# Kernel tuning notes

Hardware: AMD Instinct MI355X
Metric: run time of the kernel (lower is better)

## Reference

```python
import jax, jax.numpy as jnp
import numpy as np

B, L, E, H = 4, 2048, 1024, 16
DK = E // H


def setup_inputs() -> dict:
    key = jax.random.key(0)
    k1, k2, k3 = jax.random.split(key, 3)
    x = jax.random.normal(k1, (B, L, E), dtype=jnp.float32)
    # torch Linear weights are [out, in]; xavier-ish scaling
    w_qkv = jax.random.normal(k2, (3 * E, E), dtype=jnp.float32) * (2.0 / (E + 3 * E)) ** 0.5
    wo = jax.random.normal(k3, (E, E), dtype=jnp.float32) * (1.0 / E) ** 0.5
    # causal mask: scores filled with -inf where mask == 0
    mask = jnp.tril(jnp.ones((L, L), dtype=bool))
    return {"x": x, "mask": mask, "w_qkv": w_qkv, "wo": wo}


def reference(x, mask, w_qkv, wo):
    b, l, e = x.shape
    # qkv projection: Linear with weight [3E, E] -> x @ W^T
    qkv = x @ w_qkv.T                              # [b, l, 3E]
    qkv = qkv.reshape(b, l, 3, H, DK)              # (three h d) split
    q = jnp.transpose(qkv[:, :, 0], (0, 2, 1, 3))  # [b, h, l, d]
    k = jnp.transpose(qkv[:, :, 1], (0, 2, 1, 3))
    v = jnp.transpose(qkv[:, :, 2], (0, 2, 1, 3))
    scores = jnp.einsum('bhld,bhmd->bhlm', q, k) / np.sqrt(DK)  # [b, h, l, l]
    scores = jnp.where(mask, scores, -jnp.inf)
    attn = jax.nn.softmax(scores, axis=-1)
    out = jnp.einsum('bhlm,bhmd->bhld', attn, v)   # [b, h, l, d]
    out = jnp.transpose(out, (0, 2, 1, 3)).reshape(b, l, e)  # b l (h d)
    return out @ wo.T
```

## Files before the change

### kernel.cpp

```cpp
#include <hip/hip_runtime.h>
#include <stdint.h>


typedef __bf16 bf16;
typedef __bf16 bf16x4 __attribute__((ext_vector_type(4)));
typedef __bf16 bf16x8 __attribute__((ext_vector_type(8)));
typedef float floatx4 __attribute__((ext_vector_type(4)));
typedef short s16x4 __attribute__((ext_vector_type(4)));

#define MFMA32(a, b, c) __builtin_amdgcn_mfma_f32_16x16x32_bf16(a, b, c, 0, 0, 0)
#define MFMA16(a, b, c) __builtin_amdgcn_mfma_f32_16x16x16bf16_1k(a, b, c, 0, 0, 0)

typedef const __attribute__((address_space(1))) uint32_t* gas_t;
typedef __attribute__((address_space(3))) uint32_t* las_t;

__device__ __forceinline__ void async16(void* lds, const void* g) {
  __builtin_amdgcn_global_load_lds((gas_t)g, (las_t)lds, 16, 0, 0);
}

__global__ void cvt_all(const float4* __restrict__ x, const float4* __restrict__ wq,
                        const float4* __restrict__ wo, bf16x4* __restrict__ xb,
                        bf16x4* __restrict__ wqb, bf16x4* __restrict__ wob) {
  const int NX = 2097152, NQ = 786432;
  int i = blockIdx.x * blockDim.x + threadIdx.x;
  float4 v;
  bf16x4* dst;
  int j;
  if (i < NX) { j = i; v = x[j]; dst = xb; }
  else if (i < NX + NQ) { j = i - NX; v = wq[j]; dst = wqb; }
  else { j = i - NX - NQ; v = wo[j]; dst = wob; }
  bf16x4 o;
  o[0] = (bf16)v.x; o[1] = (bf16)v.y; o[2] = (bf16)v.z; o[3] = (bf16)v.w;
  dst[j] = o;
}

template <int MODE>
__global__ __launch_bounds__(256) void gemm_bt(
    const bf16* __restrict__ A, const bf16* __restrict__ B,
    float* __restrict__ Cf, bf16* __restrict__ Qb, bf16* __restrict__ Kb,
    bf16* __restrict__ Vt, int M, int N, int K) {
  __shared__ __align__(16) bf16 smem[128 * 136];
  bf16* As = smem;
  bf16* Bs = smem + 128 * 32;
  const int tid = threadIdx.x;
  const int wave = tid >> 6, lane = tid & 63;
  const int wm = wave & 1, wn = wave >> 1;
  const int row0 = blockIdx.y * 128, col0 = blockIdx.x * 128;
  const int l15 = lane & 15, quad = lane >> 4;
  const int srow = lane >> 2;
  const int scol = (lane & 3) * 8;

  floatx4 acc[4][4] = {};

  for (int k0 = 0; k0 < K; k0 += 32) {
#pragma unroll
    for (int i = 0; i < 2; ++i) {
      int c = wave + i * 4;
      async16(&As[c * 512], A + (size_t)(row0 + c * 16 + srow) * K + k0 + scol);
      async16(&Bs[c * 512], B + (size_t)(col0 + c * 16 + srow) * K + k0 + scol);
    }
    __syncthreads();
    bf16x8 af[4], bfr[4];
#pragma unroll
    for (int t = 0; t < 4; ++t) {
      af[t]  = *(const bf16x8*)&As[(wm * 64 + t * 16 + l15) * 32 + quad * 8];
      bfr[t] = *(const bf16x8*)&Bs[(wn * 64 + t * 16 + l15) * 32 + quad * 8];
    }
#pragma unroll
    for (int mt = 0; mt < 4; ++mt)
#pragma unroll
      for (int nt = 0; nt < 4; ++nt)
        acc[mt][nt] = MFMA32(af[mt], bfr[nt], acc[mt][nt]);
    __syncthreads();
  }

  if (MODE == 1 && col0 >= 2048) {
#pragma unroll
    for (int mt = 0; mt < 4; ++mt)
#pragma unroll
      for (int nt = 0; nt < 4; ++nt) {
        int nl = wn * 64 + nt * 16 + l15;
        int ll = wm * 64 + mt * 16 + quad * 4;
        bf16x4 t;
#pragma unroll
        for (int r = 0; r < 4; ++r) t[r] = (bf16)acc[mt][nt][r];
        *(bf16x4*)&smem[nl * 136 + ll] = t;
      }
    __syncthreads();
    const int bb = row0 >> 11, l_base = row0 & 2047, hd0 = col0 - 2048;
#pragma unroll
    for (int it = 0; it < 8; ++it) {
      int rowi = it * 16 + (tid >> 4);
      int li = (tid & 15) * 8;
      bf16x8 v = *(const bf16x8*)&smem[rowi * 136 + li];
      int hd = hd0 + rowi;
      *(bf16x8*)&Vt[((((size_t)bb * 16 + (hd >> 6)) * 64 + (hd & 63)) << 11) +
                    l_base + li] = v;
    }
    return;
  }

#pragma unroll
  for (int mt = 0; mt < 4; ++mt)
#pragma unroll
    for (int nt = 0; nt < 4; ++nt)
#pragma unroll
      for (int r = 0; r < 4; ++r) {
        int gr = row0 + wm * 64 + mt * 16 + quad * 4 + r;
        int gc = col0 + wn * 64 + nt * 16 + l15;
        float v = acc[mt][nt][r];
        if (MODE == 2) {
          Cf[(size_t)gr * N + gc] = v;
        } else {
          int t = gc >> 10, hd = gc & 1023;
          if (t == 0) Qb[(size_t)gr * 1024 + hd] = (bf16)v;
          else        Kb[(size_t)gr * 1024 + hd] = (bf16)v;
        }
      }
}

__global__ __launch_bounds__(256) void gemm2_64(
    const bf16* __restrict__ A, const bf16* __restrict__ B,
    float* __restrict__ Cf, int M, int N, int K) {
  __shared__ __align__(16) bf16 As[64 * 32];
  __shared__ __align__(16) bf16 Bs[128 * 32];
  const int tid = threadIdx.x;
  const int wave = tid >> 6, lane = tid & 63;
  const int row0 = blockIdx.y * 64, col0 = blockIdx.x * 128;
  const int l15 = lane & 15, quad = lane >> 4;
  const int srow = lane >> 2, scol = (lane & 3) * 8;

  floatx4 acc[4][2] = {};

  for (int k0 = 0; k0 < K; k0 += 32) {
#pragma unroll
    for (int i = 0; i < 3; ++i) {
      int c = wave * 3 + i;
      if (c < 4)
        async16(&As[c * 512], A + (size_t)(row0 + c * 16 + srow) * K + k0 + scol);
      else
        async16(&Bs[(c - 4) * 512],
                B + (size_t)(col0 + (c - 4) * 16 + srow) * K + k0 + scol);
    }
    __syncthreads();
    bf16x8 af[4], bfr[2];
#pragma unroll
    for (int t = 0; t < 4; ++t)
      af[t] = *(const bf16x8*)&As[(t * 16 + l15) * 32 + quad * 8];
#pragma unroll
    for (int t = 0; t < 2; ++t)
      bfr[t] = *(const bf16x8*)&Bs[(wave * 32 + t * 16 + l15) * 32 + quad * 8];
#pragma unroll
    for (int mt = 0; mt < 4; ++mt)
#pragma unroll
      for (int nt = 0; nt < 2; ++nt)
        acc[mt][nt] = MFMA32(af[mt], bfr[nt], acc[mt][nt]);
    __syncthreads();
  }

#pragma unroll
  for (int mt = 0; mt < 4; ++mt)
#pragma unroll
    for (int nt = 0; nt < 2; ++nt)
#pragma unroll
      for (int r = 0; r < 4; ++r) {
        int gr = row0 + mt * 16 + quad * 4 + r;
        int gc = col0 + wave * 32 + nt * 16 + l15;
        Cf[(size_t)gr * N + gc] = acc[mt][nt][r];
      }
}

__global__ __launch_bounds__(256, 2) void flash_attn(
    const bf16* __restrict__ Qb, const bf16* __restrict__ Kb,
    const bf16* __restrict__ Vt, bf16* __restrict__ Ob) {
  const int bid0 = blockIdx.x;
  const int xcd = bid0 & 7, jj = bid0 >> 3;
  const int bh = xcd * 8 + (jj & 7);
  const int pr = jj >> 3;
  const int b = bh >> 4, h = bh & 15;
  const int tid = threadIdx.x;
  const int wave = tid >> 6, lane = tid & 63;
  const int l15 = lane & 15, quad = lane >> 4;

  const int qA = pr, qB = 31 - pr;

  __shared__ __align__(16) bf16 Ks2[2 * 64 * 64];
  __shared__ __align__(16) bf16 Vs2[2 * 64 * 64];

  const size_t x_base = (size_t)b * 2048 * 1024 + (size_t)h * 64;
  const size_t vt_base = (size_t)bh * 64 * 2048;

  const int k_lr = lane >> 3, k_c = lane & 7;

  auto stage = [&](int kt, int bufsel) {
    bf16* Kd = Ks2 + bufsel * 4096;
    bf16* Vd = Vs2 + bufsel * 4096;
#pragma unroll
    for (int i = 0; i < 2; ++i) {
      int o8 = wave * 2 + i;
      int row = o8 * 8 + k_lr;
      int sw = (k_c ^ (row & 7)) << 3;
      async16(&Kd[o8 * 512],
              Kb + x_base + (size_t)(kt * 64 + row) * 1024 + sw);
      async16(&Vd[o8 * 512],
              Vt + vt_base + (size_t)row * 2048 + kt * 64 + sw);
    }
  };

  auto load_q = [&](int q64, bf16x8* qf) {
#pragma unroll
    for (int ks = 0; ks < 2; ++ks) {
      const bf16* p = Qb + x_base +
          (size_t)(q64 * 64 + wave * 16 + l15) * 1024 + ks * 32 + quad * 8;
      bf16x8 v = *(const bf16x8*)p;
#pragma unroll
      for (int j = 0; j < 8; ++j) v[j] = (bf16)((float)v[j] * 0.18033688f);
      qf[ks] = v;
    }
  };

  stage(0, 0);

  bf16x8 qfA[2], qfB[2];
  load_q(qA, qfA);
  load_q(qB, qfB);

  floatx4 oA[4] = {}, oB[4] = {};
  float lA = 0.f, lB = 0.f;

  auto process = [&](const bf16x8* qf, floatx4* o, float& l_run,
                     int kt, int q64, bool diag, const bf16* Ks, const bf16* Vs) {
    floatx4 s[4] = {};
    __builtin_amdgcn_s_setprio(1);
#pragma unroll
    for (int nt = 0; nt < 4; ++nt) {
      int krow = nt * 16 + l15;
#pragma unroll
      for (int ks = 0; ks < 2; ++ks) {
        bf16x8 kf = *(const bf16x8*)&Ks[krow * 64 +
            ((((ks << 2) | quad) ^ (l15 & 7)) << 3)];
        s[nt] = MFMA32(kf, qf[ks], s[nt]);
      }
    }
    __builtin_amdgcn_s_setprio(0);
    if (diag) {
      int q_g = q64 * 64 + wave * 16 + l15;
#pragma unroll
      for (int nt = 0; nt < 4; ++nt)
#pragma unroll
        for (int r = 0; r < 4; ++r)
          if (kt * 64 + nt * 16 + quad * 4 + r > q_g) s[nt][r] = -__builtin_inff();
    }
    float ls = 0.f;
#pragma unroll
    for (int nt = 0; nt < 4; ++nt)
#pragma unroll
      for (int r = 0; r < 4; ++r) {
        float p = exp2f(s[nt][r]);
        s[nt][r] = p;
        ls += p;
      }
    l_run += ls;

    __builtin_amdgcn_s_setprio(1);
#pragma unroll
    for (int kb = 0; kb < 4; ++kb) {
      bf16x4 pb;
#pragma unroll
      for (int r = 0; r < 4; ++r) pb[r] = (bf16)s[kb][r];
      s16x4 pf = __builtin_bit_cast(s16x4, pb);
#pragma unroll
      for (int dt = 0; dt < 4; ++dt) {
        s16x4 vf = *(const s16x4*)&Vs[(dt * 16 + l15) * 64 +
            (((((kb << 1) | (quad >> 1)) ^ (l15 & 7))) << 3) + ((quad & 1) << 2)];
        o[dt] = MFMA16(vf, pf, o[dt]);
      }
    }
    __builtin_amdgcn_s_setprio(0);
  };

  __syncthreads();

  int cur = 0;
  for (int kt = 0; kt <= qB; ++kt) {
    if (kt < qB) stage(kt + 1, cur ^ 1);
    const bf16* Kc = Ks2 + cur * 4096;
    const bf16* Vc = Vs2 + cur * 4096;
    process(qfB, oB, lB, kt, qB, kt == qB, Kc, Vc);
    if (kt <= qA) process(qfA, oA, lA, kt, qA, kt == qA, Kc, Vc);
    __syncthreads();
    cur ^= 1;
  }

  auto store_o = [&](const floatx4* o, float l_run, int q64) {
    float lf = l_run;
    lf += __shfl_xor(lf, 16);
    lf += __shfl_xor(lf, 32);
    float inv = 1.0f / lf;
    size_t rowoff = x_base + (size_t)(q64 * 64 + wave * 16 + l15) * 1024;
#pragma unroll
    for (int dt = 0; dt < 4; ++dt) {
      bf16x4 ob;
#pragma unroll
      for (int r = 0; r < 4; ++r) ob[r] = (bf16)(o[dt][r] * inv);
      *(bf16x4*)(Ob + rowoff + dt * 16 + quad * 4) = ob;
    }
  };
  store_o(oA, lA, qA);
  store_o(oB, lB, qB);
}

extern "C" void kernel_launch(void* const* d_in, const int* in_sizes, int n_in,
                              void* d_out, int out_size, void* d_ws, size_t ws_size,
                              hipStream_t stream) {
  const float* x     = (const float*)d_in[0];
  const float* w_qkv = (const float*)d_in[2];
  const float* wo    = (const float*)d_in[3];
  float* out = (float*)d_out;

  char* ws = (char*)d_ws;
  bf16* xb  = (bf16*)(ws);
  bf16* wqb = (bf16*)(ws + (16u << 20));
  bf16* wob = (bf16*)(ws + (22u << 20));
  bf16* Qb  = (bf16*)(ws + (24u << 20));
  bf16* Kb  = (bf16*)(ws + (40u << 20));
  bf16* Vt  = (bf16*)(ws + (56u << 20));
  bf16* Ab  = (bf16*)(ws);

  cvt_all<<<12288, 256, 0, stream>>>((const float4*)x, (const float4*)w_qkv,
                                     (const float4*)wo, (bf16x4*)xb,
                                     (bf16x4*)wqb, (bf16x4*)wob);

  gemm_bt<1><<<dim3(24, 64), 256, 0, stream>>>(xb, wqb, nullptr, Qb, Kb, Vt,
                                               8192, 3072, 1024);
  flash_attn<<<1024, 256, 0, stream>>>(Qb, Kb, Vt, Ab);
  gemm2_64<<<dim3(8, 128), 256, 0, stream>>>(Ab, wob, out, 8192, 1024, 1024);
}
```

Measured before the change: 274.7 us.

## Rewrite QKV projection GEMM with double-buffered swizzled LDS and larger tiles

Replaces the simple QKV GEMM with a 256x128-tile, 512-thread kernel. It uses K-steps of 64, a double-buffered LDS pipeline driven by async global-to-LDS loads with manual vmcnt waits, an XOR-swizzled LDS layout to avoid bank conflicts, and s_setprio around the MFMA blocks. Block IDs are remapped so each XCD handles contiguous M tiles, aiming for better L2 reuse. The goal is to hide load latency behind MFMA work and cut barrier stalls, at the cost of more LDS (96KB per block) and tighter occupancy.

Result: faster. 266.5 us (-3.0%).

```diff
diff --git a/kernel.cpp b/kernel.cpp
--- a/kernel.cpp
+++ b/kernel.cpp
@@ -34,89 +34,143 @@
   dst[j] = o;
 }
 
-template <int MODE>
-__global__ __launch_bounds__(256) void gemm_bt(
+__global__ __launch_bounds__(512, 2) void gemm_qkv(
     const bf16* __restrict__ A, const bf16* __restrict__ B,
-    float* __restrict__ Cf, bf16* __restrict__ Qb, bf16* __restrict__ Kb,
-    bf16* __restrict__ Vt, int M, int N, int K) {
-  __shared__ __align__(16) bf16 smem[128 * 136];
-  bf16* As = smem;
-  bf16* Bs = smem + 128 * 32;
+    bf16* __restrict__ Qb, bf16* __restrict__ Kb, bf16* __restrict__ Vt) {
+  __shared__ __align__(16) bf16 lds[2 * 24576];
   const int tid = threadIdx.x;
   const int wave = tid >> 6, lane = tid & 63;
-  const int wm = wave & 1, wn = wave >> 1;
-  const int row0 = blockIdx.y * 128, col0 = blockIdx.x * 128;
+  const int wr = wave >> 1, wc = wave & 1;
   const int l15 = lane & 15, quad = lane >> 4;
-  const int srow = lane >> 2;
-  const int scol = (lane & 3) * 8;
+
+  const int bid = blockIdx.x;
+  const int xcd = bid & 7, j = bid >> 3;
+  const int mt_i = xcd * 4 + (j / 24);
+  const int nt_i = j % 24;
+  const int m0 = mt_i * 256, n0 = nt_i * 128;
+
+  const int s_r = lane >> 3, s_c = lane & 7;
+
+  auto unit = [&](bf16* dst, const bf16* src) {
+#pragma unroll
+    for (int i = 0; i < 2; ++i) {
+      int g = wave * 2 + i;
+      int row = g * 8 + s_r;
+      async16(&dst[g * 512], src + (size_t)row * 1024 + ((s_c ^ (row & 7)) << 3));
+    }
+  };
+
+  const bf16* Asrc = A + (size_t)m0 * 1024;
+  const bf16* Bsrc = B + (size_t)n0 * 1024;
+
+  auto rdA = [&](const bf16* cb, int mt, int kk) -> bf16x8 {
+    int row = wr * 64 + mt * 16 + l15;
+    return *(const bf16x8*)&cb[row * 64 + ((((kk << 2) | quad) ^ (l15 & 7)) << 3)];
+  };
+  auto rdB = [&](const bf16* cb, int nt, int kk) -> bf16x8 {
+    int row = wc * 64 + nt * 16 + l15;
+    return *(const bf16x8*)&cb[16384 + row * 64 +
+                               ((((kk << 2) | quad) ^ (l15 & 7)) << 3)];
+  };
 
   floatx4 acc[4][4] = {};
 
-  for (int k0 = 0; k0 < K; k0 += 32) {
-#pragma unroll
-    for (int i = 0; i < 2; ++i) {
-      int c = wave + i * 4;
-      async16(&As[c * 512], A + (size_t)(row0 + c * 16 + srow) * K + k0 + scol);
-      async16(&Bs[c * 512], B + (size_t)(col0 + c * 16 + srow) * K + k0 + scol);
-    }
-    __syncthreads();
-    bf16x8 af[4], bfr[4];
-#pragma unroll
-    for (int t = 0; t < 4; ++t) {
-      af[t]  = *(const bf16x8*)&As[(wm * 64 + t * 16 + l15) * 32 + quad * 8];
-      bfr[t] = *(const bf16x8*)&Bs[(wn * 64 + t * 16 + l15) * 32 + quad * 8];
-    }
+  unit(lds,         Asrc);
+  unit(lds + 8192,  Asrc + (size_t)128 * 1024);
+  unit(lds + 16384, Bsrc);
+
+  auto body = [&](int t, bf16* cb, bf16* nb) {
+    const int k1 = (t + 1) << 6;
+    const bool pre = (t + 1) < 16;
+    if (pre) {
+      unit(nb, Asrc + k1);
+      asm volatile("s_waitcnt vmcnt(2)" ::: "memory");
+    } else {
+      asm volatile("s_waitcnt vmcnt(0)" ::: "memory");
+    }
+    __builtin_amdgcn_s_barrier();
+    asm volatile("" ::: "memory");
+    bf16x8 bfr[4][2];
+#pragma unroll
+    for (int nt = 0; nt < 4; ++nt)
+#pragma unroll
+      for (int kk = 0; kk < 2; ++kk) bfr[nt][kk] = rdB(cb, nt, kk);
+    bf16x8 af[2][2];
+#pragma unroll
+    for (int mt = 0; mt < 2; ++mt)
+#pragma unroll
+      for (int kk = 0; kk < 2; ++kk) af[mt][kk] = rdA(cb, mt, kk);
+    __builtin_amdgcn_s_setprio(1);
+#pragma unroll
+    for (int mt = 0; mt < 2; ++mt)
+#pragma unroll
+      for (int nt = 0; nt < 4; ++nt)
+#pragma unroll
+        for (int kk = 0; kk < 2; ++kk)
+          acc[mt][nt] = MFMA32(af[mt][kk], bfr[nt][kk], acc[mt][nt]);
+    __builtin_amdgcn_s_setprio(0);
+    if (pre) unit(nb + 8192, Asrc + (size_t)128 * 1024 + k1);
+#pragma unroll
+    for (int mt = 0; mt < 2; ++mt)
+#pragma unroll
+      for (int kk = 0; kk < 2; ++kk) af[mt][kk] = rdA(cb, mt + 2, kk);
+    if (pre) unit(nb + 16384, Bsrc + k1);
+    __builtin_amdgcn_s_setprio(1);
+#pragma unroll
+    for (int mt = 0; mt < 2; ++mt)
+#pragma unroll
+      for (int nt = 0; nt < 4; ++nt)
+#pragma unroll
+        for (int kk = 0; kk < 2; ++kk)
+          acc[mt + 2][nt] = MFMA32(af[mt][kk], bfr[nt][kk], acc[mt + 2][nt]);
+    __builtin_amdgcn_s_setprio(0);
+    __builtin_amdgcn_s_barrier();
+    asm volatile("" ::: "memory");
+  };
+
+  for (int tt = 0; tt < 8; ++tt) {
+    body(2 * tt,     lds,         lds + 24576);
+    body(2 * tt + 1, lds + 24576, lds);
+  }
+
+  if (n0 < 2048) {
+    bf16* outp = (n0 < 1024) ? Qb : Kb;
+    const int hd0 = n0 & 1023;
 #pragma unroll
     for (int mt = 0; mt < 4; ++mt)
 #pragma unroll
       for (int nt = 0; nt < 4; ++nt)
-        acc[mt][nt] = MFMA32(af[mt], bfr[nt], acc[mt][nt]);
-    __syncthreads();
-  }
-
-  if (MODE == 1 && col0 >= 2048) {
-#pragma unroll
-    for (int mt = 0; mt < 4; ++mt)
-#pragma unroll
-      for (int nt = 0; nt < 4; ++nt) {
-        int nl = wn * 64 + nt * 16 + l15;
-        int ll = wm * 64 + mt * 16 + quad * 4;
-        bf16x4 t;
-#pragma unroll
-        for (int r = 0; r < 4; ++r) t[r] = (bf16)acc[mt][nt][r];
-        *(bf16x4*)&smem[nl * 136 + ll] = t;
-      }
-    __syncthreads();
-    const int bb = row0 >> 11, l_base = row0 & 2047, hd0 = col0 - 2048;
-#pragma unroll
-    for (int it = 0; it < 8; ++it) {
-      int rowi = it * 16 + (tid >> 4);
-      int li = (tid & 15) * 8;
-      bf16x8 v = *(const bf16x8*)&smem[rowi * 136 + li];
-      int hd = hd0 + rowi;
-      *(bf16x8*)&Vt[((((size_t)bb * 16 + (hd >> 6)) * 64 + (hd & 63)) << 11) +
-                    l_base + li] = v;
-    }
+#pragma unroll
+        for (int r = 0; r < 4; ++r) {
+          int gm = m0 + wr * 64 + mt * 16 + quad * 4 + r;
+          int gh = hd0 + wc * 64 + nt * 16 + l15;
+          outp[(size_t)gm * 1024 + gh] = (bf16)acc[mt][nt][r];
+        }
     return;
   }
-
+  const int hd0 = n0 - 2048;
+  const int bb = m0 >> 11, l_base = m0 & 2047;
 #pragma unroll
   for (int mt = 0; mt < 4; ++mt)
 #pragma unroll
-    for (int nt = 0; nt < 4; ++nt)
-#pragma unroll
-      for (int r = 0; r < 4; ++r) {
-        int gr = row0 + wm * 64 + mt * 16 + quad * 4 + r;
-        int gc = col0 + wn * 64 + nt * 16 + l15;
-        float v = acc[mt][nt][r];
-        if (MODE == 2) {
-          Cf[(size_t)gr * N + gc] = v;
-        } else {
-          int t = gc >> 10, hd = gc & 1023;
-          if (t == 0) Qb[(size_t)gr * 1024 + hd] = (bf16)v;
-          else        Kb[(size_t)gr * 1024 + hd] = (bf16)v;
-        }
-      }
+    for (int nt = 0; nt < 4; ++nt) {
+      int hd_l = wc * 64 + nt * 16 + l15;
+      int l_l = wr * 64 + mt * 16 + quad * 4;
+      bf16x4 tv;
+#pragma unroll
+      for (int r = 0; r < 4; ++r) tv[r] = (bf16)acc[mt][nt][r];
+      *(bf16x4*)&lds[hd_l * 264 + l_l] = tv;
+    }
+  __syncthreads();
+  const int rr = tid >> 5, cc = tid & 31;
+#pragma unroll
+  for (int it = 0; it < 8; ++it) {
+    int row = it * 16 + rr;
+    bf16x8 v = *(const bf16x8*)&lds[row * 264 + cc * 8];
+    int hd = hd0 + row;
+    *(bf16x8*)&Vt[((((size_t)bb * 16 + (hd >> 6)) * 64 + (hd & 63)) << 11) +
+                  l_base + cc * 8] = v;
+  }
 }
 
 __global__ __launch_bounds__(256) void gemm2_64(
@@ -331,8 +385,7 @@
                                      (const float4*)wo, (bf16x4*)xb,
                                      (bf16x4*)wqb, (bf16x4*)wob);
 
-  gemm_bt<1><<<dim3(24, 64), 256, 0, stream>>>(xb, wqb, nullptr, Qb, Kb, Vt,
-                                               8192, 3072, 1024);
+  gemm_qkv<<<768, 512, 0, stream>>>(xb, wqb, Qb, Kb, Vt);
   flash_attn<<<1024, 256, 0, stream>>>(Qb, Kb, Vt, Ab);
   gemm2_64<<<dim3(8, 128), 256, 0, stream>>>(Ab, wob, out, 8192, 1024, 1024);
 }
```
